# Kernel optimization log

Measured on AMD Instinct MI355X. Metric: run time of the kernel, lower is better.

The kernel has to match this reference:

```python
import jax, jax.numpy as jnp
import numpy as np
import math

C = 128
LAM = 0.25
MARGIN = 0.3
TAU = math.log(C)
B = 8192


def lambertw(z, iters=10):
    """Principal-branch Lambert W via Halley iterations (valid for z >= -1/e)."""
    e = jnp.exp(1.0)
    # series init near the branch point z = -1/e, log init for z >= 0
    p = jnp.sqrt(jnp.maximum(2.0 * (e * z + 1.0), 0.0))
    w_near = -1.0 + p - p * p / 3.0 + (11.0 / 72.0) * p ** 3
    w = jnp.where(z < 0.0, w_near, jnp.log1p(jnp.maximum(z, 0.0)))
    for _ in range(iters):
        ew = jnp.exp(w)
        f = w * ew - z
        wp1 = w + 1.0
        w = w - f / (ew * wp1 - (w + 2.0) * f / (2.0 * wp1))
    return w


def triplet_loss(x, targets):
    # pairwise euclidean distances [B, B]
    sq = jnp.sum(x * x, axis=1)
    dist = sq[:, None] + sq[None, :] - 2.0 * (x @ x.T)
    dist = jnp.sqrt(jnp.maximum(dist, 1e-12))
    pos = targets[:, None] == targets[None, :]
    # hardest positive / hardest negative per anchor
    dist_ap = jnp.max(jnp.where(pos, dist, -jnp.inf), axis=1)
    dist_an = jnp.min(jnp.where(pos, jnp.inf, dist), axis=1)
    # MarginRankingLoss(margin)(dist_an, dist_ap, y=1), mean reduction
    return jnp.mean(jnp.maximum(dist_ap - dist_an + MARGIN, 0.0))


def cross_entropy(logits, targets):
    logp = jax.nn.log_softmax(logits, axis=-1)
    return -jnp.mean(jnp.take_along_axis(logp, targets[:, None], axis=1)[:, 0])


def setup_inputs() -> dict:
    key = jax.random.key(0)
    k1, k2 = jax.random.split(key)
    logits = jax.random.normal(k1, (B, C), dtype=jnp.float32)
    targets = jax.random.randint(k2, (B,), 0, C, dtype=jnp.int64)
    return {"logits": logits, "targets": targets}


def reference(logits, targets):
    # l_i is detached in the original (and sigma goes through numpy -> no grad)
    l_i = jax.lax.stop_gradient(triplet_loss(logits, targets))
    y = 0.5 * jnp.maximum(-2.0 / jnp.exp(1.0), (l_i - TAU) / LAM)
    sigma = jax.lax.stop_gradient(jnp.exp(-lambertw(y)))
    ce = cross_entropy(logits, targets)
    loss = (ce - TAU) * sigma + LAM * jnp.log(sigma) ** 2
    return jnp.sum(loss) / B
```

## Files before the change

kernel.cpp:

```cpp
#include <hip/hip_runtime.h>
#include <math.h>

#define NB 8192
#define NC 128
#define NJS 8
#define JPT 8

typedef float v4f __attribute__((ext_vector_type(4)));
typedef int   v8i __attribute__((ext_vector_type(8)));


__global__ __launch_bounds__(256) void k_prep(const float* __restrict__ x,
                                              const int* __restrict__ tgt,
                                              unsigned* __restrict__ xq,
                                              float* __restrict__ sq,
                                              float* __restrict__ ce,
                                              unsigned* __restrict__ ctl) {
    int row = blockIdx.x * 8 + (threadIdx.x >> 5);
    int l = threadIdx.x & 31;
    float4 v = ((const float4*)(x + row * NC))[l];
    unsigned p = __builtin_amdgcn_cvt_pk_fp8_f32(v.x, v.y, 0, false);
    p = __builtin_amdgcn_cvt_pk_fp8_f32(v.z, v.w, p, true);
    xq[row * 32 + l] = p;

    float ss = fmaf(v.x, v.x, fmaf(v.y, v.y, fmaf(v.z, v.z, v.w * v.w)));
    float mx = fmaxf(fmaxf(v.x, v.y), fmaxf(v.z, v.w));
#pragma unroll
    for (int off = 16; off; off >>= 1) {
        ss += __shfl_xor(ss, off);
        mx = fmaxf(mx, __shfl_xor(mx, off));
    }
    float es = expf(v.x - mx) + expf(v.y - mx) + expf(v.z - mx) + expf(v.w - mx);
#pragma unroll
    for (int off = 16; off; off >>= 1) es += __shfl_xor(es, off);
    if (l == 0) {
        sq[row] = ss;
        ce[row] = mx + logf(es) - x[row * NC + tgt[row]];
    }
    if (blockIdx.x == 0) {
        uint4 zz = {0u, 0u, 0u, 0u};
#pragma unroll
        for (int k = 0; k < 8; ++k)
            ((uint4*)ctl)[threadIdx.x + k * 256] = zz;
    }
}

__global__ __launch_bounds__(256, 4) void k_trip(const unsigned char* __restrict__ xq,
                                                 const int* __restrict__ tgt,
                                                 const float* __restrict__ sq,
                                                 const float* __restrict__ ce,
                                                 unsigned* __restrict__ ctl,
                                                 float* __restrict__ pmax,
                                                 float* __restrict__ pmin,
                                                 float* __restrict__ out) {
    __shared__ union {
        struct { unsigned char Bs[2][128 * 128]; float sqs[1024]; int tjs[1024]; } p2;
        struct { unsigned doTail; } p3;
    } sm;

    const int tid = threadIdx.x;
    const int lane = tid & 63;
    const int w = tid >> 6;
    const int rh = w >> 1;
    const int ch = w & 1;
    const int bx = (int)blockIdx.x;
    const int by = (int)blockIdx.y;
    const int i0 = bx * 64;
    const int jbase = by * 1024;
    const int m = lane & 15;
    const int quad = lane >> 4;

    __builtin_amdgcn_global_load_lds(
        (const __attribute__((address_space(1))) unsigned*)((const unsigned*)(sq + jbase) + (w * 64 + lane) * 4),
        (__attribute__((address_space(3))) unsigned*)(sm.p2.sqs + w * 256),
        16, 0, 0);
    __builtin_amdgcn_global_load_lds(
        (const __attribute__((address_space(1))) unsigned*)((const unsigned*)(tgt + jbase) + (w * 64 + lane) * 4),
        (__attribute__((address_space(3))) unsigned*)(sm.p2.tjs + w * 256),
        16, 0, 0);

#pragma unroll
    for (int c = 0; c < 4; ++c) {
        int L = w * 256 + c * 64 + lane;
        int col = L >> 3, cc = L & 7;
        const unsigned char* src = xq + (size_t)(jbase + col) * 128 + ((cc ^ (col & 7)) << 4);
        __builtin_amdgcn_global_load_lds(
            (const __attribute__((address_space(1))) unsigned*)src,
            (__attribute__((address_space(3))) unsigned*)(&sm.p2.Bs[0][0] + (w * 256 + c * 64) * 16),
            16, 0, 0);
    }

    v8i a[2];
#pragma unroll
    for (int tm = 0; tm < 2; ++tm) {
        int row = i0 + rh * 32 + tm * 16 + m;
        a[tm] = *(const v8i*)(xq + (size_t)row * 128 + quad * 32);
    }

    int ti[2][4];
#pragma unroll
    for (int tm = 0; tm < 2; ++tm)
#pragma unroll
        for (int r = 0; r < 4; ++r)
            ti[tm][r] = tgt[i0 + rh * 32 + tm * 16 + quad * 4 + r];

    float mp[2][4], mn[2][4];
#pragma unroll
    for (int tm = 0; tm < 2; ++tm)
#pragma unroll
        for (int r = 0; r < 4; ++r) { mp[tm][r] = -3.0e38f; mn[tm][r] = 3.0e38f; }

#pragma unroll 2
    for (int jt = 0; jt < JPT; ++jt) {
        __syncthreads();

        if (jt + 1 < JPT) {
            int jn = jbase + (jt + 1) * 128;
            unsigned char* Bnxt = &sm.p2.Bs[(jt + 1) & 1][0];
#pragma unroll
            for (int c = 0; c < 4; ++c) {
                int L = w * 256 + c * 64 + lane;
                int col = L >> 3, cc = L & 7;
                const unsigned char* src = xq + (size_t)(jn + col) * 128 + ((cc ^ (col & 7)) << 4);
                __builtin_amdgcn_global_load_lds(
                    (const __attribute__((address_space(1))) unsigned*)src,
                    (__attribute__((address_space(3))) unsigned*)(Bnxt + (w * 256 + c * 64) * 16),
                    16, 0, 0);
            }
        }

        const unsigned char* Bcur = &sm.p2.Bs[jt & 1][0];

        float sqj[4]; int tj[4];
#pragma unroll
        for (int tn = 0; tn < 4; ++tn) {
            int cloc = jt * 128 + ch * 64 + tn * 16 + m;
            sqj[tn] = sm.p2.sqs[cloc];
            tj[tn] = sm.p2.tjs[cloc];
        }

        v8i b[4];
#pragma unroll
        for (int tn = 0; tn < 4; ++tn) {
            int col = ch * 64 + tn * 16 + m;
            int base = col * 128;
            int c0 = (((quad * 2) ^ (col & 7)) << 4);
            int c1 = (((quad * 2 + 1) ^ (col & 7)) << 4);
            *(int4*)&b[tn] = *(const int4*)(Bcur + base + c0);
            *((int4*)&b[tn] + 1) = *(const int4*)(Bcur + base + c1);
        }

        v4f acc[2][4];
        v4f z = {0.0f, 0.0f, 0.0f, 0.0f};
#pragma unroll
        for (int tm = 0; tm < 2; ++tm)
#pragma unroll
            for (int tn = 0; tn < 4; ++tn)
                acc[tm][tn] = __builtin_amdgcn_mfma_scale_f32_16x16x128_f8f6f4(
                    a[tm], b[tn], z, 0, 0, 0, 0x7f7f7f7f, 0, 0x7f7f7f7f);

#pragma unroll
        for (int tn = 0; tn < 4; ++tn) {
#pragma unroll
            for (int tm = 0; tm < 2; ++tm)
#pragma unroll
                for (int r = 0; r < 4; ++r) {
                    float v = fmaf(-2.0f, acc[tm][tn][r], sqj[tn]);
                    bool pos = (tj[tn] == ti[tm][r]);
                    mp[tm][r] = fmaxf(mp[tm][r], pos ? v : -3.0e38f);
                    mn[tm][r] = fminf(mn[tm][r], pos ? 3.0e38f : v);
                }
        }
    }

#pragma unroll
    for (int off = 1; off < 16; off <<= 1) {
#pragma unroll
        for (int tm = 0; tm < 2; ++tm)
#pragma unroll
            for (int r = 0; r < 4; ++r) {
                mp[tm][r] = fmaxf(mp[tm][r], __shfl_xor(mp[tm][r], off));
                mn[tm][r] = fminf(mn[tm][r], __shfl_xor(mn[tm][r], off));
            }
    }
    if (m == 0) {
        int slice = by * 2 + ch;
        float* pm = pmax + (size_t)slice * NB + i0 + rh * 32;
        float* pn = pmin + (size_t)slice * NB + i0 + rh * 32;
#pragma unroll
        for (int tm = 0; tm < 2; ++tm)
#pragma unroll
            for (int r = 0; r < 4; ++r) {
                int rr = tm * 16 + quad * 4 + r;
                __hip_atomic_store(pm + rr, mp[tm][r], __ATOMIC_RELAXED, __HIP_MEMORY_SCOPE_AGENT);
                __hip_atomic_store(pn + rr, mn[tm][r], __ATOMIC_RELAXED, __HIP_MEMORY_SCOPE_AGENT);
            }
    }

    __syncthreads();
    if (tid == 0) {
        unsigned prev = __hip_atomic_fetch_add(ctl + (16u + (unsigned)bx) * 32, 1u,
                                               __ATOMIC_RELAXED, __HIP_MEMORY_SCOPE_AGENT);
        sm.p3.doTail = (prev == 7u);
    }
    __syncthreads();
    if (!sm.p3.doTail) return;

    if (tid < 64) {
        int i = i0 + tid;
        float vmax = -3.0e38f, vmin = 3.0e38f;
#pragma unroll
        for (int s = 0; s < 16; ++s) {
            vmax = fmaxf(vmax, __hip_atomic_load(pmax + (size_t)s * NB + i,
                                                 __ATOMIC_RELAXED, __HIP_MEMORY_SCOPE_AGENT));
            vmin = fminf(vmin, __hip_atomic_load(pmin + (size_t)s * NB + i,
                                                 __ATOMIC_RELAXED, __HIP_MEMORY_SCOPE_AGENT));
        }
        float sqi = sq[i];
        float ap = sqrtf(fmaxf(fmaxf(sqi + vmax, 0.0f), 1e-12f));
        float an = sqrtf(fmaxf(fmaxf(sqi + vmin, 0.0f), 1e-12f));
        float hs = fmaxf(ap - an + 0.3f, 0.0f);
        float cs = ce[i];
#pragma unroll
        for (int off = 32; off; off >>= 1) {
            hs += __shfl_xor(hs, off);
            cs += __shfl_xor(cs, off);
        }
        if (tid == 0) {
            float* pl = (float*)(ctl + (8u + (unsigned)(bx & 7)) * 32);
            atomicAdd(pl + 0, hs);
            atomicAdd(pl + 1, cs);
            asm volatile("s_waitcnt vmcnt(0)" ::: "memory");
            unsigned prev2 = __hip_atomic_fetch_add(ctl + 0, 1u,
                                                    __ATOMIC_RELAXED, __HIP_MEMORY_SCOPE_AGENT);
            if (prev2 == 127u) {
                double H = 0.0, Cs = 0.0;
#pragma unroll
                for (int k = 0; k < 8; ++k) {
                    float* q = (float*)(ctl + (8u + (unsigned)k) * 32);
                    H  += (double)atomicAdd(q + 0, 0.0f);
                    Cs += (double)atomicAdd(q + 1, 0.0f);
                }
                const double E = 2.71828182845904523536;
                const double TAU = log(128.0);
                const double LAMd = 0.25;
                double l = H / (double)NB;
                double cev = Cs / (double)NB;
                double y = 0.5 * fmax(-2.0 / E, (l - TAU) / LAMd);
                double p = sqrt(fmax(2.0 * (E * y + 1.0), 0.0));
                double wn = -1.0 + p - p * p / 3.0 + (11.0 / 72.0) * p * p * p;
                double wlw = (y < 0.0) ? wn : log1p(fmax(y, 0.0));
#pragma unroll
                for (int it = 0; it < 10; ++it) {
                    double ew = exp(wlw);
                    double f = wlw * ew - y;
                    double wp1 = wlw + 1.0;
                    wlw = wlw - f / (ew * wp1 - (wlw + 2.0) * f / (2.0 * wp1));
                }
                double sigma = exp(-wlw);
                double lg = log(sigma);
                double loss = (cev - TAU) * sigma + LAMd * lg * lg;
                out[0] = (float)(loss / (double)NB);
            }
        }
    }
}

extern "C" void kernel_launch(void* const* d_in, const int* in_sizes, int n_in,
                              void* d_out, int out_size, void* d_ws, size_t ws_size,
                              hipStream_t stream) {
    const float* x = (const float*)d_in[0];
    const int* tgt = (const int*)d_in[1];
    float* out = (float*)d_out;

    unsigned char* xq = (unsigned char*)d_ws;
    float* sq = (float*)(xq + (size_t)NB * 128);
    float* ce = sq + NB;
    unsigned* ctl = (unsigned*)(ce + NB);
    float* pmax = (float*)((unsigned char*)ctl + 32768);
    float* pmin = pmax + (size_t)16 * NB;

    k_prep<<<NB / 8, 256, 0, stream>>>(x, tgt, (unsigned*)xq, sq, ce, ctl);
    dim3 grid(NB / 64, NJS);
    k_trip<<<grid, 256, 0, stream>>>(xq, tgt, sq, ce, ctl, pmax, pmin, out);
}
```

Measured before the change: 86.64 us.

## Split j-range into 16 slices with smaller tiles and parallel tail reduction

Doubles the number of column slices so each block covers 512 columns in 64-column tiles. This halves LDS usage and raises the occupancy hint to 8 blocks per CU, giving twice as many blocks to hide latency and balance load. The tail merge now reads 32 partial slices, so all four waves share the reads and reduce through shared memory instead of one wave reading serially. The cost is twice as many partial-result writes and counter atomics, and fewer MFMAs per B-tile load.

```diff
diff --git a/kernel.cpp b/kernel.cpp
--- a/kernel.cpp
+++ b/kernel.cpp
@@ -3,12 +3,21 @@
 
 #define NB 8192
 #define NC 128
-#define NJS 8
+#define NJS 16
 #define JPT 8
+#define NSL 32
 
 typedef float v4f __attribute__((ext_vector_type(4)));
 typedef int   v8i __attribute__((ext_vector_type(8)));
 
+
+
+__device__ __forceinline__ float ld_f32(const float* p) {
+    return __hip_atomic_load(p, __ATOMIC_RELAXED, __HIP_MEMORY_SCOPE_AGENT);
+}
+__device__ __forceinline__ void st_f32(float* p, float v) {
+    __hip_atomic_store(p, v, __ATOMIC_RELAXED, __HIP_MEMORY_SCOPE_AGENT);
+}
 
 __global__ __launch_bounds__(256) void k_prep(const float* __restrict__ x,
                                               const int* __restrict__ tgt,
@@ -45,7 +54,7 @@
     }
 }
 
-__global__ __launch_bounds__(256, 4) void k_trip(const unsigned char* __restrict__ xq,
+__global__ __launch_bounds__(256, 8) void k_trip(const unsigned char* __restrict__ xq,
                                                  const int* __restrict__ tgt,
                                                  const float* __restrict__ sq,
                                                  const float* __restrict__ ce,
@@ -54,8 +63,8 @@
                                                  float* __restrict__ pmin,
                                                  float* __restrict__ out) {
     __shared__ union {
-        struct { unsigned char Bs[2][128 * 128]; float sqs[1024]; int tjs[1024]; } p2;
-        struct { unsigned doTail; } p3;
+        struct { unsigned char Bs[2][64 * 128]; float sqs[512]; int tjs[512]; } p2;
+        struct { unsigned doTail; float vmx[4][64]; float vmn[4][64]; } p3;
     } sm;
 
     const int tid = threadIdx.x;
@@ -66,27 +75,30 @@
     const int bx = (int)blockIdx.x;
     const int by = (int)blockIdx.y;
     const int i0 = bx * 64;
-    const int jbase = by * 1024;
+    const int jbase = by * 512;
     const int m = lane & 15;
     const int quad = lane >> 4;
 
-    __builtin_amdgcn_global_load_lds(
-        (const __attribute__((address_space(1))) unsigned*)((const unsigned*)(sq + jbase) + (w * 64 + lane) * 4),
-        (__attribute__((address_space(3))) unsigned*)(sm.p2.sqs + w * 256),
-        16, 0, 0);
-    __builtin_amdgcn_global_load_lds(
-        (const __attribute__((address_space(1))) unsigned*)((const unsigned*)(tgt + jbase) + (w * 64 + lane) * 4),
-        (__attribute__((address_space(3))) unsigned*)(sm.p2.tjs + w * 256),
-        16, 0, 0);
-
-#pragma unroll
-    for (int c = 0; c < 4; ++c) {
-        int L = w * 256 + c * 64 + lane;
+    if (w < 2) {
+        __builtin_amdgcn_global_load_lds(
+            (const __attribute__((address_space(1))) unsigned*)((const unsigned*)(sq + jbase) + (w * 64 + lane) * 4),
+            (__attribute__((address_space(3))) unsigned*)(sm.p2.sqs + w * 256),
+            16, 0, 0);
+    } else {
+        __builtin_amdgcn_global_load_lds(
+            (const __attribute__((address_space(1))) unsigned*)((const unsigned*)(tgt + jbase) + ((w - 2) * 64 + lane) * 4),
+            (__attribute__((address_space(3))) unsigned*)(sm.p2.tjs + (w - 2) * 256),
+            16, 0, 0);
+    }
+
+#pragma unroll
+    for (int c = 0; c < 2; ++c) {
+        int L = w * 128 + c * 64 + lane;
         int col = L >> 3, cc = L & 7;
         const unsigned char* src = xq + (size_t)(jbase + col) * 128 + ((cc ^ (col & 7)) << 4);
         __builtin_amdgcn_global_load_lds(
             (const __attribute__((address_space(1))) unsigned*)src,
-            (__attribute__((address_space(3))) unsigned*)(&sm.p2.Bs[0][0] + (w * 256 + c * 64) * 16),
+            (__attribute__((address_space(3))) unsigned*)(&sm.p2.Bs[0][0] + (w * 128 + c * 64) * 16),
             16, 0, 0);
     }
 
@@ -115,34 +127,34 @@
         __syncthreads();
 
         if (jt + 1 < JPT) {
-            int jn = jbase + (jt + 1) * 128;
+            int jn = jbase + (jt + 1) * 64;
             unsigned char* Bnxt = &sm.p2.Bs[(jt + 1) & 1][0];
 #pragma unroll
-            for (int c = 0; c < 4; ++c) {
-                int L = w * 256 + c * 64 + lane;
+            for (int c = 0; c < 2; ++c) {
+                int L = w * 128 + c * 64 + lane;
                 int col = L >> 3, cc = L & 7;
                 const unsigned char* src = xq + (size_t)(jn + col) * 128 + ((cc ^ (col & 7)) << 4);
                 __builtin_amdgcn_global_load_lds(
                     (const __attribute__((address_space(1))) unsigned*)src,
-                    (__attribute__((address_space(3))) unsigned*)(Bnxt + (w * 256 + c * 64) * 16),
+                    (__attribute__((address_space(3))) unsigned*)(Bnxt + (w * 128 + c * 64) * 16),
                     16, 0, 0);
             }
         }
 
         const unsigned char* Bcur = &sm.p2.Bs[jt & 1][0];
 
-        float sqj[4]; int tj[4];
-#pragma unroll
-        for (int tn = 0; tn < 4; ++tn) {
-            int cloc = jt * 128 + ch * 64 + tn * 16 + m;
+        float sqj[2]; int tj[2];
+#pragma unroll
+        for (int tn = 0; tn < 2; ++tn) {
+            int cloc = jt * 64 + ch * 32 + tn * 16 + m;
             sqj[tn] = sm.p2.sqs[cloc];
             tj[tn] = sm.p2.tjs[cloc];
         }
 
-        v8i b[4];
-#pragma unroll
-        for (int tn = 0; tn < 4; ++tn) {
-            int col = ch * 64 + tn * 16 + m;
+        v8i b[2];
+#pragma unroll
+        for (int tn = 0; tn < 2; ++tn) {
+            int col = ch * 32 + tn * 16 + m;
             int base = col * 128;
             int c0 = (((quad * 2) ^ (col & 7)) << 4);
             int c1 = (((quad * 2 + 1) ^ (col & 7)) << 4);
@@ -150,17 +162,17 @@
             *((int4*)&b[tn] + 1) = *(const int4*)(Bcur + base + c1);
         }
 
-        v4f acc[2][4];
+        v4f acc[2][2];
         v4f z = {0.0f, 0.0f, 0.0f, 0.0f};
 #pragma unroll
         for (int tm = 0; tm < 2; ++tm)
 #pragma unroll
-            for (int tn = 0; tn < 4; ++tn)
+            for (int tn = 0; tn < 2; ++tn)
                 acc[tm][tn] = __builtin_amdgcn_mfma_scale_f32_16x16x128_f8f6f4(
                     a[tm], b[tn], z, 0, 0, 0, 0x7f7f7f7f, 0, 0x7f7f7f7f);
 
 #pragma unroll
-        for (int tn = 0; tn < 4; ++tn) {
+        for (int tn = 0; tn < 2; ++tn) {
 #pragma unroll
             for (int tm = 0; tm < 2; ++tm)
 #pragma unroll
@@ -192,8 +204,8 @@
 #pragma unroll
             for (int r = 0; r < 4; ++r) {
                 int rr = tm * 16 + quad * 4 + r;
-                __hip_atomic_store(pm + rr, mp[tm][r], __ATOMIC_RELAXED, __HIP_MEMORY_SCOPE_AGENT);
-                __hip_atomic_store(pn + rr, mn[tm][r], __ATOMIC_RELAXED, __HIP_MEMORY_SCOPE_AGENT);
+                st_f32(pm + rr, mp[tm][r]);
+                st_f32(pn + rr, mn[tm][r]);
             }
     }
 
@@ -201,21 +213,31 @@
     if (tid == 0) {
         unsigned prev = __hip_atomic_fetch_add(ctl + (16u + (unsigned)bx) * 32, 1u,
                                                __ATOMIC_RELAXED, __HIP_MEMORY_SCOPE_AGENT);
-        sm.p3.doTail = (prev == 7u);
+        sm.p3.doTail = (prev == (unsigned)(NJS - 1));
     }
     __syncthreads();
     if (!sm.p3.doTail) return;
 
+    {
+        int lr = tid & 63, g = tid >> 6;
+        int i = i0 + lr;
+        float vmax = -3.0e38f, vmin = 3.0e38f;
+#pragma unroll
+        for (int k = 0; k < 8; ++k) {
+            int s = g * 8 + k;
+            vmax = fmaxf(vmax, ld_f32(pmax + (size_t)s * NB + i));
+            vmin = fminf(vmin, ld_f32(pmin + (size_t)s * NB + i));
+        }
+        sm.p3.vmx[g][lr] = vmax;
+        sm.p3.vmn[g][lr] = vmin;
+    }
+    __syncthreads();
     if (tid < 64) {
         int i = i0 + tid;
-        float vmax = -3.0e38f, vmin = 3.0e38f;
-#pragma unroll
-        for (int s = 0; s < 16; ++s) {
-            vmax = fmaxf(vmax, __hip_atomic_load(pmax + (size_t)s * NB + i,
-                                                 __ATOMIC_RELAXED, __HIP_MEMORY_SCOPE_AGENT));
-            vmin = fminf(vmin, __hip_atomic_load(pmin + (size_t)s * NB + i,
-                                                 __ATOMIC_RELAXED, __HIP_MEMORY_SCOPE_AGENT));
-        }
+        float vmax = fmaxf(fmaxf(sm.p3.vmx[0][tid], sm.p3.vmx[1][tid]),
+                           fmaxf(sm.p3.vmx[2][tid], sm.p3.vmx[3][tid]));
+        float vmin = fminf(fminf(sm.p3.vmn[0][tid], sm.p3.vmn[1][tid]),
+                           fminf(sm.p3.vmn[2][tid], sm.p3.vmn[3][tid]));
         float sqi = sq[i];
         float ap = sqrtf(fmaxf(fmaxf(sqi + vmax, 0.0f), 1e-12f));
         float an = sqrtf(fmaxf(fmaxf(sqi + vmin, 0.0f), 1e-12f));
@@ -278,7 +300,7 @@
     float* ce = sq + NB;
     unsigned* ctl = (unsigned*)(ce + NB);
     float* pmax = (float*)((unsigned char*)ctl + 32768);
-    float* pmin = pmax + (size_t)16 * NB;
+    float* pmin = pmax + (size_t)NSL * NB;
 
     k_prep<<<NB / 8, 256, 0, stream>>>(x, tgt, (unsigned*)xq, sq, ce, ctl);
     dim3 grid(NB / 64, NJS);
```

Result: slower. 171.3 us (+97.7%).
